# Kernel optimization log

Hardware: AMD Instinct MI355X
Metric: run time of the kernel (lower is better)

The kernel has to match this reference:

```python
import jax, jax.numpy as jnp
import numpy as np

N_SAMPLES, N_ASSETS = 64, 256
N_CLUSTERS, N_INIT, MAX_ITER = 8, 10, 30
SEED = 42


def cov2corr(cov):
    d = jnp.sqrt(jnp.diagonal(cov, axis1=-2, axis2=-1))
    return cov / (d[..., :, None] * d[..., None, :])


def kmeans_single(x, key):
    # x: (n, d) points; Lloyd's algorithm, 'random' init (pick n_clusters points).
    n = x.shape[0]
    idx = jax.random.choice(key, n, (N_CLUSTERS,), replace=False)
    centers0 = x[idx]

    def step(centers, _):
        d2 = ((x[:, None, :] - centers[None, :, :]) ** 2).sum(-1)  # (n, k)
        ixs = jnp.argmin(d2, axis=1)
        onehot = jax.nn.one_hot(ixs, N_CLUSTERS, dtype=x.dtype)    # (n, k)
        counts = onehot.sum(0)
        new_centers = (onehot.T @ x) / jnp.maximum(counts, 1.0)[:, None]
        new_centers = jnp.where(counts[:, None] > 0, new_centers, centers)
        return new_centers, None

    centers, _ = jax.lax.scan(step, centers0, None, length=MAX_ITER)
    d2 = ((x[:, None, :] - centers[None, :, :]) ** 2).sum(-1)
    ixs = jnp.argmin(d2, axis=1)
    inertia = jnp.min(d2, axis=1).sum()
    return ixs, inertia


def cluster_weights(mask, cov, r):
    # Masked-block analytical Markowitz: solving the system with identity on the
    # off-cluster block and zero RHS is exactly the sub-matrix solve of the original.
    n = cov.shape[0]
    eye = jnp.eye(n, dtype=cov.dtype)
    m2 = mask[:, None] & mask[None, :]
    A = jnp.where(m2, cov, eye)
    b = jnp.where(mask, r, 0.0)
    w = jnp.linalg.solve(A, b)          # zeros outside cluster by construction
    denom = w.sum()                     # = ones^T Sigma_c^{-1} mu_c
    return jnp.where(denom != 0, w / denom, 0.0)


def nco_sample(cov, r, key):
    corr = cov2corr(cov)
    keys = jax.random.split(key, N_INIT)
    ixs_all, inertia = jax.vmap(lambda k: kmeans_single(corr, k))(keys)
    ixs = jax.lax.stop_gradient(ixs_all[jnp.argmin(inertia)])      # (n,)
    masks = ixs[None, :] == jnp.arange(N_CLUSTERS)[:, None]        # (k, n)
    w_cols = jax.vmap(cluster_weights, in_axes=(0, None, None))(masks, cov, r)  # (k, n)
    w_intra = w_cols.T                                             # (n, k)
    inter_cov = w_intra.T @ cov @ w_intra                          # (k, k)
    inter_rets = w_intra.T @ r                                     # (k,)
    w_u = jnp.linalg.solve(inter_cov, inter_rets)
    w_inter = w_u / w_u.sum()
    return w_intra @ w_inter                                       # (n,)


def setup_inputs() -> dict:
    key = jax.random.key(0)
    k1, k2 = jax.random.split(key)
    # SPD covariance: factor model + diagonal jitter
    F = jax.random.normal(k1, (N_SAMPLES, N_ASSETS, N_ASSETS), dtype=jnp.float32)
    covmat = jnp.einsum('bij,bkj->bik', F, F) / N_ASSETS \
        + 0.1 * jnp.eye(N_ASSETS, dtype=jnp.float32)[None]
    rets = jax.random.uniform(k2, (N_SAMPLES, N_ASSETS), dtype=jnp.float32,
                              minval=0.01, maxval=1.0)
    return {"covmat": covmat, "rets": rets}


def reference(covmat, rets):
    base = jax.random.key(SEED)
    keys = jax.random.split(base, covmat.shape[0])
    return jax.vmap(nco_sample)(covmat, rets, keys)  # (n_samples, n_assets)
```

## Files before the change

### kernel.cpp

```cpp
#include <hip/hip_runtime.h>
#include <stdint.h>

#define NS 64
#define NA 256
#define NC 8
#define NI 10
#define MAXIT 30
#define MLDS 90

typedef unsigned int u32;
typedef unsigned long long u64;

struct Key { u32 x, y; };

__device__ __forceinline__ void tf2x32(u32 k0, u32 k1, u32 c0, u32 c1, u32& o0, u32& o1) {
  u32 ks0 = k0, ks1 = k1, ks2 = k0 ^ k1 ^ 0x1BD11BDAu;
  u32 x0 = c0 + ks0, x1 = c1 + ks1;
#define TFR(r) { x0 += x1; x1 = (x1 << (r)) | (x1 >> (32 - (r))); x1 ^= x0; }
  TFR(13) TFR(15) TFR(26) TFR(6)
  x0 += ks1; x1 += ks2 + 1u;
  TFR(17) TFR(29) TFR(16) TFR(24)
  x0 += ks2; x1 += ks0 + 2u;
  TFR(13) TFR(15) TFR(26) TFR(6)
  x0 += ks0; x1 += ks1 + 3u;
  TFR(17) TFR(29) TFR(16) TFR(24)
  x0 += ks1; x1 += ks2 + 4u;
  TFR(13) TFR(15) TFR(26) TFR(6)
  x0 += ks2; x1 += ks0 + 5u;
#undef TFR
  o0 = x0; o1 = x1;
}

__device__ __forceinline__ Key key_row(Key k, u32 j) {
  Key r; tf2x32(k.x, k.y, 0u, j, r.x, r.y); return r;
}
__device__ __forceinline__ u32 rbits32(Key k, u32 i) {
  u32 o0, o1; tf2x32(k.x, k.y, 0u, i, o0, o1); return o0 ^ o1;
}

__global__ __launch_bounds__(256) void nco_gram_kernel(
    const float* __restrict__ cov, double* __restrict__ G) {
  int b = blockIdx.x;
  int j = b / 10, tile = b - 10 * j;
  const int TIa[10] = {0,0,0,0,1,1,1,2,2,3};
  const int TJa[10] = {0,1,2,3,1,2,3,2,3,3};
  int ti2 = TIa[tile], tj2 = TJa[tile];
  const float* C = cov + (size_t)j * NA * NA;
  double* Gj = G + (size_t)j * NA * NA;

  __shared__ double sinv[NA];
  __shared__ double As[16][64 + 1];
  __shared__ double Bs[16][64 + 1];
  int t = threadIdx.x;
  int tr = t >> 4, tc = t & 15;

  sinv[t] = 1.0 / sqrt((double)C[(size_t)t * NA + t]);
  __syncthreads();

  double acc[4][4];
#pragma unroll
  for (int a = 0; a < 4; a++)
#pragma unroll
    for (int bb = 0; bb < 4; bb++) acc[a][bb] = 0.0;

  for (int k0 = 0; k0 < NA; k0 += 16) {
    int kk = t & 15, rr = t >> 4;
    double ck = sinv[k0 + kk];
#pragma unroll
    for (int m = 0; m < 4; m++) {
      int r = rr + 16 * m;
      int gr = ti2 * 64 + r;
      As[kk][r] = (double)C[(size_t)gr * NA + k0 + kk] * sinv[gr] * ck;
      int gc = tj2 * 64 + r;
      Bs[kk][r] = (double)C[(size_t)gc * NA + k0 + kk] * sinv[gc] * ck;
    }
    __syncthreads();
#pragma unroll
    for (int kk2 = 0; kk2 < 16; kk2++) {
      double ar[4], br[4];
#pragma unroll
      for (int m = 0; m < 4; m++) ar[m] = As[kk2][tr + 16 * m];
#pragma unroll
      for (int m = 0; m < 4; m++) br[m] = Bs[kk2][tc + 16 * m];
#pragma unroll
      for (int a = 0; a < 4; a++)
#pragma unroll
        for (int bb = 0; bb < 4; bb++) acc[a][bb] = fma(ar[a], br[bb], acc[a][bb]);
    }
    __syncthreads();
  }
#pragma unroll
  for (int a = 0; a < 4; a++) {
    int gr = ti2 * 64 + tr + 16 * a;
#pragma unroll
    for (int bb = 0; bb < 4; bb++) {
      int gc = tj2 * 64 + tc + 16 * bb;
      Gj[(size_t)gr * NA + gc] = acc[a][bb];
      if (ti2 != tj2) Gj[(size_t)gc * NA + gr] = acc[a][bb];
    }
  }
}

__global__ __launch_bounds__(512) void nco_kmeans_kernel(
    const double* __restrict__ G, int* __restrict__ ixsAll,
    double* __restrict__ inertiaAll) {
  int b = blockIdx.x;
  int xcd = b & 7, s0 = b >> 3;
  int j  = xcd + 8 * (s0 / NI);
  int mi = s0 - (s0 / NI) * NI;
  int blk = j * NI + mi;
  int tid = threadIdx.x;
  int t = tid & 255;
  int g = tid >> 8;
  int w4 = tid >> 6;
  const double* Gj = G + (size_t)j * NA * NA;

  __shared__ int    li[NC][NA];
  __shared__ double sv[NC][NA];
  __shared__ int    wcnt[4][NC];
  __shared__ u64    balPrev[4][NC];
  __shared__ u64    balNew[4][NC];
  __shared__ u64    dAdd[4][NC];
  __shared__ u64    dRem[4][NC];
  __shared__ int    nsz[NC];
  __shared__ int    dirty[NC];
  __shared__ double part[NC][8];
  __shared__ double sinvn[NC], ck2[NC];
  __shared__ u32    bits[NA];

  if (g == 0) {
    Key base; base.x = 0u; base.y = 42u;
    Key skey = key_row(base, (u32)j);
    Key ikey = key_row(skey, (u32)mi);
    Key sub  = key_row(ikey, 1u);
    bits[t] = rbits32(sub, (u32)t);
  }
  __syncthreads();
  if (g == 0) {
    u32 mine = bits[t];
    int rank = 0;
    for (int u = 0; u < NA; u++) {
      u32 b2 = bits[u];
      rank += (b2 < mine) || (b2 == mine && u < t);
    }
    if (rank < NC) li[rank][0] = t;
    if (t < NC) { nsz[t] = 1; dirty[t] = 1; }
#pragma unroll
    for (int k = 0; k < NC; k++) {
      u64 bal = __ballot(rank == k);
      if ((t & 63) == 0) balPrev[w4][k] = bal;
    }
  }
  __syncthreads();

  double xx = (g == 0) ? Gj[(size_t)t * NA + t] : 0.0;
  int myix = -1;
  double fb = 0.0;
  for (int it = 0; it <= MAXIT; ++it) {
    if (it > 0) {
      u64 mybal = 0;
      if (g == 0) {
#pragma unroll
        for (int k = 0; k < NC; k++) {
          u64 bal = __ballot(myix == k);
          if ((t & 63) == 0) { wcnt[w4][k] = (int)__popcll(bal); balNew[w4][k] = bal; }
          if (k == myix) mybal = bal;
        }
      }
      __syncthreads();
      if (g == 0) {
        if (t < NC) {
          int tot = wcnt[0][t] + wcnt[1][t] + wcnt[2][t] + wcnt[3][t];
          if (tot > 0) {
            nsz[t] = tot;
            bool d = (balNew[0][t] != balPrev[0][t]) | (balNew[1][t] != balPrev[1][t]) |
                     (balNew[2][t] != balPrev[2][t]) | (balNew[3][t] != balPrev[3][t]);
            dirty[t] = d ? 1 : 0;
            if (d) {
#pragma unroll
              for (int w2 = 0; w2 < 4; w2++) {
                dAdd[w2][t] = balNew[w2][t] & ~balPrev[w2][t];
                dRem[w2][t] = balPrev[w2][t] & ~balNew[w2][t];
                balPrev[w2][t] = balNew[w2][t];
              }
            }
          } else {
            dirty[t] = 0;
          }
        }
        int k = myix;
        int base = 0;
        for (int w2 = 0; w2 < w4; w2++) base += wcnt[w2][k];
        li[k][base + (int)__popcll(mybal & ((1ULL << (t & 63)) - 1ULL))] = t;
      }
      __syncthreads();
      if (!(dirty[0] | dirty[1] | dirty[2] | dirty[3] |
            dirty[4] | dirty[5] | dirty[6] | dirty[7])) break;

      for (int k = g; k < NC; k += 2) {
        if (!dirty[k]) continue;
        double acc = sv[k][t];
#pragma unroll
        for (int wq = 0; wq < 4; wq++) {
          u64 m0 = dRem[wq][k];
          while (m0) {
            int p = (wq << 6) + (int)__builtin_ctzll(m0);
            m0 &= m0 - 1;
            acc -= Gj[(size_t)p * NA + t];
          }
        }
#pragma unroll
        for (int wq = 0; wq < 4; wq++) {
          u64 m0 = dAdd[wq][k];
          while (m0) {
            int p = (wq << 6) + (int)__builtin_ctzll(m0);
            m0 &= m0 - 1;
            acc += Gj[(size_t)p * NA + t];
          }
        }
        sv[k][t] = acc;
      }
    } else {
      for (int k = g; k < NC; k += 2) {
        int p = li[k][0];
        sv[k][t] = Gj[(size_t)p * NA + t];
      }
    }
    __syncthreads();

    if (tid < 64) {
      int k = tid >> 3, r = tid & 7;
      if (dirty[k]) {
        int n = nsz[k];
        double p = 0.0;
        for (int i = r; i < n; i += 8) p += sv[k][li[k][i]];
        part[k][r] = p;
      }
      __builtin_amdgcn_wave_barrier();
      if (tid < NC && dirty[tid]) {
        double S = 0.0;
#pragma unroll
        for (int r2 = 0; r2 < 8; r2++) S += part[tid][r2];
        double inn = 1.0 / (double)nsz[tid];
        sinvn[tid] = inn;
        ck2[tid] = S * inn * inn;
      }
    }
    __syncthreads();

    if (g == 0) {
      double best = ck2[0] - 2.0 * sv[0][t] * sinvn[0]; int bi = 0;
#pragma unroll
      for (int k = 1; k < NC; k++) {
        double f = ck2[k] - 2.0 * sv[k][t] * sinvn[k];
        if (f < best) { best = f; bi = k; }
      }
      fb = best;
      myix = bi;
    }
  }

  __syncthreads();
  double* red = (double*)&li[0][0];
  if (g == 0) red[t] = xx + fb;
  __syncthreads();
  if (g == 0) ixsAll[blk * NA + t] = myix;
  if (tid == 0) {
    double ss = 0.0;
    for (int i = 0; i < NA; i++) ss += red[i];
    inertiaAll[blk] = ss;
  }
}

__global__ __launch_bounds__(256) void nco_csolve_kernel(
    const float* __restrict__ cov, const float* __restrict__ rets,
    const int* __restrict__ ixsAll, const double* __restrict__ inertiaAll,
    double* __restrict__ gbuf_all, double* __restrict__ wc_all) {
  int b = blockIdx.x;
  int j = b >> 3, c = b & 7;
  int t = threadIdx.x, w = t >> 6;
  const float* C = cov + (size_t)j * NA * NA;
  const float* r = rets + (size_t)j * NA;

  __shared__ double bufl[MLDS * (MLDS + 1)];
  __shared__ int    li[NA];
  __shared__ int    wcnt[4][NC];
  __shared__ int    scnt[NC];
  __shared__ int    sbest;
  __shared__ double rhs[NA];
  __shared__ double wsub[NA];
  __shared__ double sdenom;

  if (t == 0) {
    double bv = inertiaAll[j * NI]; int bb = 0;
    for (int m = 1; m < NI; m++) {
      double v = inertiaAll[j * NI + m];
      if (v < bv) { bv = v; bb = m; }
    }
    sbest = bb;
  }
  __syncthreads();
  const int* ixs = ixsAll + (size_t)(j * NI + sbest) * NA;

  int myc = ixs[t];
  u64 mybal = 0;
#pragma unroll
  for (int u = 0; u < NC; u++) {
    u64 bal = __ballot(myc == u);
    if ((t & 63) == 0) wcnt[w][u] = (int)__popcll(bal);
    if (u == myc) mybal = bal;
  }
  __syncthreads();
  if (t < NC) scnt[t] = wcnt[0][t] + wcnt[1][t] + wcnt[2][t] + wcnt[3][t];
  __syncthreads();
  if (myc == c) {
    int base = 0;
    for (int w2 = 0; w2 < w; w2++) base += wcnt[w2][c];
    li[base + (int)__popcll(mybal & ((1ULL << (t & 63)) - 1ULL))] = t;
  }
  double* wcc = wc_all + ((size_t)j * NC + c) * NA;
  wcc[t] = 0.0;
  __syncthreads();

  int m = scnt[c];
  if (m == 0) return;

  if (m <= 64) {
    int ms = m | 1;
    for (int idx = t; idx < m * m; idx += NA) {
      int row = idx / m, col = idx - row * m;
      bufl[row * ms + col] = (double)C[(size_t)li[row] * NA + li[col]];
    }
    if (t < m) rhs[t] = (double)r[li[t]];
    __syncthreads();
    if (t < 64) {
      for (int k = 0; k < m - 1; k++) {
        double piv = bufl[k * ms + k];
        if (t > k && t < m) {
          double f = bufl[t * ms + k] / piv;
          rhs[t] -= f * rhs[k];
          for (int b2 = k + 1; b2 < m; b2++)
            bufl[t * ms + b2] -= f * bufl[k * ms + b2];
        }
        __builtin_amdgcn_wave_barrier();
      }
      for (int a = m - 1; a >= 0; a--) {
        if (t == a) wsub[a] = rhs[a] / bufl[a * ms + a];
        __builtin_amdgcn_wave_barrier();
        if (t < a) rhs[t] -= bufl[t * ms + a] * wsub[a];
        __builtin_amdgcn_wave_barrier();
      }
      double ssum = 0.0;
      for (int a = 0; a < m; a++) ssum += wsub[a];
      if (t < m) wcc[li[t]] = (ssum != 0.0) ? (wsub[t] / ssum) : 0.0;
    }
    return;
  }

  int inlds = (m <= MLDS);
  int ms = inlds ? (m | 1) : m;
  double* bp;
  if (inlds) {
    bp = bufl;
  } else {
    int soff = 0;
    for (int u = 0; u < c; u++) soff += scnt[u] * scnt[u];
    bp = gbuf_all + (size_t)j * NA * NA + soff;
  }

  for (int idx = t; idx < m * m; idx += NA) {
    int row = idx / m, col = idx - row * m;
    bp[(size_t)row * ms + col] = (double)C[(size_t)li[row] * NA + li[col]];
  }
  if (t < m) rhs[t] = (double)r[li[t]];
  __syncthreads();

  for (int k = 0; k < m - 1; k++) {
    double piv = bp[(size_t)k * ms + k];
    if (t > k && t < m) {
      double f = bp[(size_t)t * ms + k] / piv;
      rhs[t] -= f * rhs[k];
      for (int b2 = k + 1; b2 < m; b2++)
        bp[(size_t)t * ms + b2] -= f * bp[(size_t)k * ms + b2];
    }
    __syncthreads();
  }
  for (int a = m - 1; a >= 0; a--) {
    if (t == a) wsub[a] = rhs[a] / bp[(size_t)a * ms + a];
    __syncthreads();
    if (t < a) rhs[t] -= bp[(size_t)t * ms + a] * wsub[a];
    __syncthreads();
  }
  if (t == 0) {
    double ssum = 0.0;
    for (int a = 0; a < m; a++) ssum += wsub[a];
    sdenom = ssum;
  }
  __syncthreads();
  if (t < m) wcc[li[t]] = (sdenom != 0.0) ? (wsub[t] / sdenom) : 0.0;
}

__global__ __launch_bounds__(256) void nco_inter_kernel(
    const float* __restrict__ cov, const float* __restrict__ rets,
    const double* __restrict__ wc_all, float* __restrict__ out) {
  int j = blockIdx.x, t = threadIdx.x;
  const float* C = cov + (size_t)j * NA * NA;
  const float* r = rets + (size_t)j * NA;

  __shared__ double wc[NC][NA];
  __shared__ double tmpL[NC][NA];
  __shared__ double interA[NC][NC];
  __shared__ double interb[NC];
  __shared__ double wi[NC];

  for (int c = 0; c < NC; c++) wc[c][t] = wc_all[((size_t)j * NC + c) * NA + t];
  __syncthreads();

  {
    double tcol[NC];
#pragma unroll
    for (int c = 0; c < NC; c++) tcol[c] = 0.0;
    for (int p = 0; p < NA; p++) {
      double cv = (double)C[(size_t)p * NA + t];
#pragma unroll
      for (int c = 0; c < NC; c++) tcol[c] += wc[c][p] * cv;
    }
#pragma unroll
    for (int c = 0; c < NC; c++) tmpL[c][t] = tcol[c];
  }
  __syncthreads();

  if (t < NC * NC) {
    int c = t / NC, c2 = t % NC;
    double s = 0.0;
    for (int q = 0; q < NA; q++) s += tmpL[c][q] * wc[c2][q];
    interA[c][c2] = s;
  }
  if (t >= 64 && t < 64 + NC) {
    int c = t - 64;
    double s = 0.0;
    for (int p = 0; p < NA; p++) s += wc[c][p] * (double)r[p];
    interb[c] = s;
  }
  __syncthreads();

  if (t == 0) {
    double A[NC][NC], bb[NC];
    for (int a = 0; a < NC; a++) {
      bb[a] = interb[a];
      for (int q = 0; q < NC; q++) A[a][q] = interA[a][q];
    }
    for (int k = 0; k < NC; k++) {
      int p = k; double mx = fabs(A[k][k]);
      for (int i2 = k + 1; i2 < NC; i2++) {
        double v = fabs(A[i2][k]);
        if (v > mx) { mx = v; p = i2; }
      }
      if (p != k) {
        for (int q = 0; q < NC; q++) { double tv = A[k][q]; A[k][q] = A[p][q]; A[p][q] = tv; }
        double tb = bb[k]; bb[k] = bb[p]; bb[p] = tb;
      }
      for (int i2 = k + 1; i2 < NC; i2++) {
        double f = A[i2][k] / A[k][k];
        bb[i2] -= f * bb[k];
        for (int q = k + 1; q < NC; q++) A[i2][q] -= f * A[k][q];
      }
    }
    double w[NC];
    for (int a = NC - 1; a >= 0; a--) {
      double s = bb[a];
      for (int q = a + 1; q < NC; q++) s -= A[a][q] * w[q];
      w[a] = s / A[a][a];
    }
    double ssum = 0.0;
    for (int a = 0; a < NC; a++) ssum += w[a];
    for (int a = 0; a < NC; a++) wi[a] = w[a] / ssum;
  }
  __syncthreads();

  double o = 0.0;
#pragma unroll
  for (int c = 0; c < NC; c++) o += wc[c][t] * wi[c];
  out[(size_t)j * NA + t] = (float)o;
}

extern "C" void kernel_launch(void* const* d_in, const int* in_sizes, int n_in,
                              void* d_out, int out_size, void* d_ws, size_t ws_size,
                              hipStream_t stream) {
  const float* cov  = (const float*)d_in[0];
  const float* rets = (const float*)d_in[1];
  float* out = (float*)d_out;
  char* ws = (char*)d_ws;

  const size_t g_bytes = (size_t)NS * NA * NA * sizeof(double);
  double* G          = (double*)(ws);
  double* inertiaAll = (double*)(ws + g_bytes);
  int*    ixsAll     = (int*)   (ws + g_bytes + 5120);
  double* wc_all     = (double*)(ws + g_bytes + 5120 + 655360);
  double* gbuf_all   = G;

  hipLaunchKernelGGL(nco_gram_kernel,   dim3(NS * 10), dim3(NA),  0, stream, cov, G);
  hipLaunchKernelGGL(nco_kmeans_kernel, dim3(NS * NI), dim3(512), 0, stream,
                     G, ixsAll, inertiaAll);
  hipLaunchKernelGGL(nco_csolve_kernel, dim3(NS * NC), dim3(NA),  0, stream,
                     cov, rets, ixsAll, inertiaAll, gbuf_all, wc_all);
  hipLaunchKernelGGL(nco_inter_kernel,  dim3(NS),      dim3(NA),  0, stream,
                     cov, rets, wc_all, out);
}
```

Measured before the change: 309.1 us.

## Parallelize Gaussian elimination over submatrix elements and single-wave back-substitution

The elimination step previously had one thread per row loop serially over columns. Now the row multipliers are computed first, then all elements of the trailing submatrix are updated in parallel across the block, at the cost of an extra block barrier per pivot. Back-substitution now runs in a single 64-thread wave using wave barriers instead of block-wide __syncthreads, and the denominator is summed inside that wave. This targets the path for larger clusters, both when the matrix fits in LDS and when it spills to global memory.

```diff
diff --git a/kernel.cpp b/kernel.cpp
--- a/kernel.cpp
+++ b/kernel.cpp
@@ -289,7 +289,7 @@
   __shared__ int    sbest;
   __shared__ double rhs[NA];
   __shared__ double wsub[NA];
-  __shared__ double sdenom;
+  __shared__ double fv[NA];
 
   if (t == 0) {
     double bv = inertiaAll[j * NI]; int bb = 0;
@@ -358,7 +358,7 @@
   }
 
   int inlds = (m <= MLDS);
-  int ms = inlds ? (m | 1) : m;
+  int msl = inlds ? (m | 1) : m;
   double* bp;
   if (inlds) {
     bp = bufl;
@@ -370,34 +370,42 @@
 
   for (int idx = t; idx < m * m; idx += NA) {
     int row = idx / m, col = idx - row * m;
-    bp[(size_t)row * ms + col] = (double)C[(size_t)li[row] * NA + li[col]];
+    bp[(size_t)row * msl + col] = (double)C[(size_t)li[row] * NA + li[col]];
   }
   if (t < m) rhs[t] = (double)r[li[t]];
   __syncthreads();
 
   for (int k = 0; k < m - 1; k++) {
-    double piv = bp[(size_t)k * ms + k];
-    if (t > k && t < m) {
-      double f = bp[(size_t)t * ms + k] / piv;
-      rhs[t] -= f * rhs[k];
-      for (int b2 = k + 1; b2 < m; b2++)
-        bp[(size_t)t * ms + b2] -= f * bp[(size_t)k * ms + b2];
-    }
-    __syncthreads();
-  }
-  for (int a = m - 1; a >= 0; a--) {
-    if (t == a) wsub[a] = rhs[a] / bp[(size_t)a * ms + a];
-    __syncthreads();
-    if (t < a) rhs[t] -= bp[(size_t)t * ms + a] * wsub[a];
-    __syncthreads();
-  }
-  if (t == 0) {
+    double piv = bp[(size_t)k * msl + k];
+    int nr = m - 1 - k;
+    if (t < nr) {
+      int row = k + 1 + t;
+      double f = bp[(size_t)row * msl + k] / piv;
+      fv[row] = f;
+      rhs[row] -= f * rhs[k];
+    }
+    __syncthreads();
+    int tot = nr * nr;
+    for (int idx = t; idx < tot; idx += NA) {
+      int rr = idx / nr, cc = idx - rr * nr;
+      int row = k + 1 + rr, col = k + 1 + cc;
+      bp[(size_t)row * msl + col] -= fv[row] * bp[(size_t)k * msl + col];
+    }
+    __syncthreads();
+  }
+
+  if (t < 64) {
+    for (int a = m - 1; a >= 0; a--) {
+      if ((a & 63) == t) wsub[a] = rhs[a] / bp[(size_t)a * msl + a];
+      __builtin_amdgcn_wave_barrier();
+      for (int r2 = t; r2 < a; r2 += 64) rhs[r2] -= bp[(size_t)r2 * msl + a] * wsub[a];
+      __builtin_amdgcn_wave_barrier();
+    }
     double ssum = 0.0;
     for (int a = 0; a < m; a++) ssum += wsub[a];
-    sdenom = ssum;
-  }
-  __syncthreads();
-  if (t < m) wcc[li[t]] = (sdenom != 0.0) ? (wsub[t] / sdenom) : 0.0;
+    for (int r2 = t; r2 < m; r2 += 64)
+      wcc[li[r2]] = (ssum != 0.0) ? (wsub[r2] / ssum) : 0.0;
+  }
 }
 
 __global__ __launch_bounds__(256) void nco_inter_kernel(
```

Result: no change. 309.3 us (+0.0%).
